# Kernel optimization log

Hardware: AMD Instinct MI355X
Metric: run time of the kernel (lower is better)

The kernel has to match this reference:

```python
import jax, jax.numpy as jnp
import numpy as np

B, N, DIM = 4, 1024, 768
HEADS, DIM_HEAD = 12, 64
INNER = HEADS * DIM_HEAD  # 768
SCALE = DIM ** -0.5


def setup_inputs() -> dict:
    key = jax.random.key(0)
    ks = jax.random.split(key, 5)
    return {
        "x": jax.random.normal(ks[0], (B, N, DIM), dtype=jnp.float32),
        "pos_embedding": jax.random.normal(ks[1], (B, N, DIM), dtype=jnp.float32),
        "w_qkv": jax.random.normal(ks[2], (DIM, 3 * INNER), dtype=jnp.float32) * (DIM ** -0.5),
        "w_qk_pos": jax.random.normal(ks[3], (DIM, 2 * INNER), dtype=jnp.float32) * (DIM ** -0.5),
        "w_out": jax.random.normal(ks[4], (INNER, DIM), dtype=jnp.float32) * (INNER ** -0.5),
        "b_out": jnp.zeros((DIM,), dtype=jnp.float32),
    }


def _split_heads(t):
    # [b, n, h*d] -> [b, h, n, d]
    b, n, _ = t.shape
    return t.reshape(b, n, HEADS, DIM_HEAD).transpose(0, 2, 1, 3)


def reference(x, pos_embedding, w_qkv, w_qk_pos, w_out, b_out):
    qkv = x @ w_qkv  # [b, n, 3*inner]
    q, k, v = (_split_heads(t) for t in jnp.split(qkv, 3, axis=-1))
    qk_pos = pos_embedding @ w_qk_pos  # [b, n, 2*inner]
    q_pos, k_pos = (_split_heads(t) for t in jnp.split(qk_pos, 2, axis=-1))

    dots = jnp.einsum('bhid,bhjd->bhij', q, k) * SCALE
    dots_pos = jnp.einsum('bhid,bhjd->bhij', q_pos, k_pos) * SCALE
    dots = (dots + dots_pos) * 0.5  # averaged content+positional scores

    attn = jax.nn.softmax(dots, axis=-1)
    out = jnp.einsum('bhij,bhjd->bhid', attn, v)
    out = out.transpose(0, 2, 1, 3).reshape(x.shape[0], x.shape[1], INNER)
    return out @ w_out + b_out
```

## Files before the change

### kernel.cpp

```cpp
#include <hip/hip_runtime.h>
#include <cstdint>
#include <cstddef>

typedef __bf16 bf16;
typedef __bf16 bf16x8 __attribute__((ext_vector_type(8)));
typedef __bf16 bf16x4v __attribute__((ext_vector_type(4)));
typedef float  f32x4  __attribute__((ext_vector_type(4)));

#define MFMA(a, b, c) __builtin_amdgcn_mfma_f32_16x16x32_bf16((a), (b), (c), 0, 0, 0)

typedef __attribute__((address_space(3))) unsigned int  lds_u32;
typedef __attribute__((address_space(1))) unsigned int glob_u32;


__global__ void k_prep(const float* __restrict__ x, const float* __restrict__ pos,
                       const float* __restrict__ w_qkv, const float* __restrict__ w_qk_pos,
                       const float* __restrict__ w_out,
                       bf16* __restrict__ xb, bf16* __restrict__ posb,
                       bf16* __restrict__ wqkvT, bf16* __restrict__ wqkposT,
                       bf16* __restrict__ woutT) {
    __shared__ float t[32][33];
    const int blk = blockIdx.x;
    if (blk < 6144) {
        int i = blk * 256 + threadIdx.x;
        const float* in = x; bf16* out = xb;
        if (i >= 786432) { i -= 786432; in = pos; out = posb; }
        float4 v = reinterpret_cast<const float4*>(in)[i];
        bf16x4v o; o[0] = (bf16)v.x; o[1] = (bf16)v.y; o[2] = (bf16)v.z; o[3] = (bf16)v.w;
        reinterpret_cast<bf16x4v*>(out)[i] = o;
        return;
    }
    int bx = (blk - 6144) % 144, ky = (blk - 6144) / 144;
    const float* in; bf16* out; int N;
    if (bx < 72)       { in = w_qkv;    out = wqkvT;   N = 2304; }
    else if (bx < 120) { in = w_qk_pos; out = wqkposT; N = 1536; bx -= 72; }
    else               { in = w_out;    out = woutT;   N = 768;  bx -= 120; }
    const int n0 = bx * 32, k0 = ky * 32;
    const int tx = threadIdx.x & 31, ty = threadIdx.x >> 5;
#pragma unroll
    for (int r = 0; r < 32; r += 8)
        t[ty + r][tx] = in[(size_t)(k0 + ty + r) * N + n0 + tx];
    __syncthreads();
#pragma unroll
    for (int r = 0; r < 32; r += 8)
        out[(size_t)(n0 + ty + r) * 768 + k0 + tx] = (bf16)t[tx][ty + r];
}

__launch_bounds__(512, 2)
__global__ void k_gemm12(const bf16* __restrict__ xb, const bf16* __restrict__ posb,
                         const bf16* __restrict__ wqkvT, const bf16* __restrict__ wqkposT,
                         bf16* __restrict__ qcat, bf16* __restrict__ kcat,
                         bf16* __restrict__ vT) {
    __shared__ bf16 lA[2][2][2][128][32];
    __shared__ bf16 lB[2][2][2][128][32];

    const int tid  = threadIdx.x;
    const int lane = tid & 63, wave = tid >> 6;
    const int quad = lane >> 4, col = lane & 15;
    const int sw2  = (col >> 1) & 3;
    const int rg8  = (quad ^ sw2) * 8;
    const int mh   = wave >> 2;
    const int nh   = (wave >> 1) & 1;
    const int nb64 = (wave & 1) * 64;
    const int wm   = mh * 128, wn = (wave & 3) * 64;

    const int fid = blockIdx.x;
    const int xcd = fid & 7, s = fid >> 3;
    const int bx = s % 15;
    const int by = xcd * 2 + s / 15;

    int mode, nBase;
    const bf16 *A, *BT;
    if (bx < 9) { mode = 0; A = xb;   BT = wqkvT;   nBase = bx * 256; }
    else        { mode = 1; A = posb; BT = wqkposT; nBase = (bx - 9) * 256; }
    const int mBase = by * 256;

    const bf16* Ap = A  + (size_t)mBase * 768;
    const bf16* Bp = BT + (size_t)nBase * 768;

#define STAGE_A8(ss, h, t)                                                     \
    _Pragma("unroll")                                                          \
    for (int j = 0; j < 2; ++j) {                                              \
        int c = (lane & 3) ^ ((lane >> 3) & 3);                                \
        __builtin_amdgcn_global_load_lds(                                      \
            (const glob_u32*)(Ap + (size_t)((h) * 128 + wave * 16 + (lane >> 2)) * 768 \
                              + (t) * 64 + j * 32 + c * 8),                    \
            (lds_u32*)(&lA[ss][h][j][wave * 16][0]), 16, 0, 0);                \
    }
#define STAGE_B8(ss, h, t)                                                     \
    _Pragma("unroll")                                                          \
    for (int j = 0; j < 2; ++j) {                                              \
        int c = (lane & 3) ^ ((lane >> 3) & 3);                                \
        __builtin_amdgcn_global_load_lds(                                      \
            (const glob_u32*)(Bp + (size_t)((h) * 128 + wave * 16 + (lane >> 2)) * 768 \
                              + (t) * 64 + j * 32 + c * 8),                    \
            (lds_u32*)(&lB[ss][h][j][wave * 16][0]), 16, 0, 0);                \
    }

#define READ_A8(ss, mq)                                                        \
    _Pragma("unroll")                                                          \
    for (int f = 0; f < 4; ++f)                                                \
    _Pragma("unroll")                                                          \
    for (int ks = 0; ks < 2; ++ks)                                             \
        afr[f][ks] = *(const bf16x8*)&lA[ss][mh][ks][(mq) * 64 + f * 16 + col][rg8];
#define READ_B8(ss, nq)                                                        \
    _Pragma("unroll")                                                          \
    for (int n = 0; n < 2; ++n)                                                \
    _Pragma("unroll")                                                          \
    for (int ks = 0; ks < 2; ++ks)                                             \
        bfr[n][ks] = *(const bf16x8*)&lB[ss][nh][ks][nb64 + (nq) * 32 + n * 16 + col][rg8];

#define MM16(mq, nq)                                                           \
    __builtin_amdgcn_s_setprio(1);                                             \
    _Pragma("unroll")                                                          \
    for (int ks = 0; ks < 2; ++ks)                                             \
    _Pragma("unroll")                                                          \
    for (int f = 0; f < 4; ++f)                                                \
    _Pragma("unroll")                                                          \
    for (int n = 0; n < 2; ++n)                                                \
        acc[(mq) * 4 + f][(nq) * 2 + n] =                                      \
            MFMA(afr[f][ks], bfr[n][ks], acc[(mq) * 4 + f][(nq) * 2 + n]);     \
    __builtin_amdgcn_s_setprio(0);

#define BAR()   __builtin_amdgcn_s_barrier()
#define LGKM0() do { asm volatile("s_waitcnt lgkmcnt(0)" ::: "memory");        \
                     __builtin_amdgcn_sched_barrier(0); } while (0)

    f32x4 acc[8][4];
#pragma unroll
    for (int mi = 0; mi < 8; ++mi)
#pragma unroll
        for (int ni = 0; ni < 4; ++ni) acc[mi][ni] = f32x4{0.f, 0.f, 0.f, 0.f};

    bf16x8 afr[4][2], bfr[2][2];

    STAGE_A8(0, 0, 0) STAGE_A8(0, 1, 0)
    STAGE_B8(0, 0, 0)
    STAGE_B8(0, 1, 0)
    STAGE_A8(1, 0, 1) STAGE_A8(1, 1, 1)
    asm volatile("s_waitcnt vmcnt(4)" ::: "memory");
    BAR();

    for (int i = 0; i < 6; ++i) {
        const int tO = 2 * i + 1, tE2 = 2 * i + 2, tO2 = 2 * i + 3;
        READ_A8(0, 0) READ_B8(0, 0)
        STAGE_B8(1, 0, tO)
        BAR(); LGKM0();
        MM16(0, 0)
        BAR();
        READ_B8(0, 1)
        STAGE_B8(1, 1, tO)
        BAR(); LGKM0();
        MM16(0, 1)
        BAR();
        READ_A8(0, 1)
        BAR(); LGKM0();
        MM16(1, 1)
        BAR();
        READ_B8(0, 0)
        if (i < 5) { STAGE_A8(0, 0, tE2) STAGE_A8(0, 1, tE2) }
        BAR(); LGKM0();
        MM16(1, 0)
        if (i < 5) { asm volatile("s_waitcnt vmcnt(4)" ::: "memory"); }
        else       { asm volatile("s_waitcnt vmcnt(0)" ::: "memory"); }
        BAR();
        READ_A8(1, 0) READ_B8(1, 0)
        if (i < 5) STAGE_B8(0, 1, tE2)
        BAR(); LGKM0();
        MM16(0, 0)
        BAR();
        READ_B8(1, 1)
        if (i < 5) STAGE_B8(0, 0, tE2)
        BAR(); LGKM0();
        MM16(0, 1)
        BAR();
        READ_A8(1, 1)
        BAR(); LGKM0();
        MM16(1, 1)
        BAR();
        READ_B8(1, 0)
        if (i < 5) { STAGE_A8(1, 0, tO2) STAGE_A8(1, 1, tO2) }
        BAR(); LGKM0();
        MM16(1, 0)
        if (i < 5) { asm volatile("s_waitcnt vmcnt(4)" ::: "memory"); }
        BAR();
    }
#undef STAGE_A8
#undef STAGE_B8
#undef READ_A8
#undef READ_B8
#undef MM16
#undef BAR
#undef LGKM0

    const float c2s = 0.018042195912f * 1.44269504089f;
    const int bb = mBase >> 10;
    const int sr0 = (mBase & 1023) + wm + quad * 4;
    const int which = (mode == 0) ? (nBase >= 1536 ? 2 : (nBase >= 768 ? 1 : 0))
                                  : (nBase >= 768 ? 1 : 0);
#pragma unroll
    for (int ni = 0; ni < 4; ++ni) {
        const int nb = nBase + wn + ni * 16;
        const int rem = nb - which * 768;
        const int hh = rem >> 6, dd0 = rem & 63;
        const size_t hb = (size_t)(bb * 12 + hh);
        if (mode == 0 && which == 2) {
            bf16* dstv = vT + (hb * 64 + dd0 + col) * 1024 + sr0;
#pragma unroll
            for (int mi = 0; mi < 8; ++mi) {
                bf16x4v pk;
#pragma unroll
                for (int r = 0; r < 4; ++r) pk[r] = (bf16)acc[mi][ni][r];
                *(bf16x4v*)(dstv + mi * 16) = pk;
            }
        } else {
            const float scl = (which == 0) ? c2s : 1.0f;
            bf16* dstq = (which == 0 ? qcat : kcat)
                       + (hb * 1024 + sr0) * 128 + (mode == 1 ? 64 : 0) + dd0 + col;
#pragma unroll
            for (int mi = 0; mi < 8; ++mi)
#pragma unroll
                for (int r = 0; r < 4; ++r)
                    dstq[(size_t)(mi * 16 + r) * 128] = (bf16)(acc[mi][ni][r] * scl);
        }
    }
}

__launch_bounds__(256, 3)
__global__ void k_attn(const bf16* __restrict__ qcat, const bf16* __restrict__ kcat,
                       const bf16* __restrict__ vT, bf16* __restrict__ attn_out) {
    __shared__ bf16 lK[2][64][128];
    __shared__ bf16 lV[2][64][72];

    const int tid  = threadIdx.x;
    const int lane = tid & 63, wave = tid >> 6;
    const int quad = lane >> 4, col = lane & 15;
    const int sw   = col & 7;

    const int fid = blockIdx.x;
    const int xcd = fid & 7, s = fid >> 3;
    const int qt = s & 15;
    const int unit = (s >> 4) * 8 + xcd;
    const int b = unit / 12, h = unit % 12;

    const bf16* Qb = qcat + (size_t)unit * 1024 * 128;
    const bf16* Kb = kcat + (size_t)unit * 1024 * 128;
    const bf16* Vb = vT   + (size_t)unit * 64 * 1024;

    const int kidx = wave * 256 + lane;

#define STAGE_K(buf, kv0)                                                      \
    _Pragma("unroll")                                                          \
    for (int j = 0; j < 4; ++j) {                                              \
        int idx = kidx + j * 64;                                               \
        int row = idx >> 4, c = idx & 15, csrc = c ^ (row & 7);                \
        __builtin_amdgcn_global_load_lds(                                      \
            (const glob_u32*)(Kb + (size_t)((kv0) + row) * 128 + csrc * 8),    \
            (lds_u32*)(&lK[buf][0][0] + (wave * 4 + j) * 512), 16, 0, 0);      \
    }

    int vdj[2], vsk[2], vka[2];
#pragma unroll
    for (int j = 0; j < 2; ++j) {
        int cid = wave * 128 + j * 64 + lane;
        vdj[j] = cid >> 3;
        int sck = cid & 7;
        vsk[j] = sck * 8;
        vka[j] = (sck >> 2) * 32 + (sck & 1) * 16 + ((sck >> 1) & 1) * 4;
    }

#define LOAD_V(kv0)                                                            \
    _Pragma("unroll")                                                          \
    for (int j = 0; j < 2; ++j)                                                \
        vreg[j] = *(const uint4*)(Vb + (size_t)vdj[j] * 1024 + (kv0) + vsk[j]);
#define WRITE_V(buf)                                                           \
    _Pragma("unroll")                                                          \
    for (int j = 0; j < 2; ++j) {                                               \
        *(uint2*)&lV[buf][vdj[j]][vka[j]]     = make_uint2(vreg[j].x, vreg[j].y);\
        *(uint2*)&lV[buf][vdj[j]][vka[j] + 8] = make_uint2(vreg[j].z, vreg[j].w);\
    }

    bf16x8 qb[4];
    {
        const bf16* qrow = Qb + (size_t)(qt * 64 + wave * 16 + col) * 128;
#pragma unroll
        for (int f = 0; f < 4; ++f) qb[f] = *(const bf16x8*)(qrow + f * 32 + quad * 8);
    }

    f32x4 o[4];
#pragma unroll
    for (int vt = 0; vt < 4; ++vt) o[vt] = f32x4{0.f, 0.f, 0.f, 0.f};
    float lsum = 0.f;

    uint4 vreg[2];
    STAGE_K(0, 0)
    LOAD_V(0)
    WRITE_V(0)

    for (int it = 0; it < 16; ++it) {
        const int cur = it & 1, nxt = cur ^ 1;
        __syncthreads();
        if (it < 15) {
            const int kv1 = (it + 1) * 64;
            STAGE_K(nxt, kv1)
            LOAD_V(kv1)
        }

        f32x4 st[4];
#pragma unroll
        for (int t = 0; t < 4; ++t) st[t] = f32x4{0.f, 0.f, 0.f, 0.f};
        __builtin_amdgcn_s_setprio(1);
#pragma unroll
        for (int t = 0; t < 4; ++t)
#pragma unroll
            for (int f = 0; f < 4; ++f) {
                bf16x8 kf = *(const bf16x8*)&lK[cur][t * 16 + col][((f * 4 + quad) ^ sw) * 8];
                st[t] = MFMA(kf, qb[f], st[t]);
            }
        __builtin_amdgcn_s_setprio(0);

        bf16x8 pbf[2];
#pragma unroll
        for (int c = 0; c < 2; ++c) {
#pragma unroll
            for (int r = 0; r < 4; ++r) {
                float p0 = exp2f(st[2 * c][r]);
                float p1 = exp2f(st[2 * c + 1][r]);
                lsum += p0 + p1;
                pbf[c][r]     = (bf16)p0;
                pbf[c][4 + r] = (bf16)p1;
            }
        }

        __builtin_amdgcn_s_setprio(1);
#pragma unroll
        for (int c = 0; c < 2; ++c)
#pragma unroll
            for (int vt = 0; vt < 4; ++vt) {
                bf16x8 vf = *(const bf16x8*)&lV[cur][vt * 16 + col][c * 32 + quad * 8];
                o[vt] = MFMA(vf, pbf[c], o[vt]);
            }
        __builtin_amdgcn_s_setprio(0);

        if (it < 15) WRITE_V(nxt)
    }

    float l = lsum;
    l += __shfl_xor(l, 16, 64);
    l += __shfl_xor(l, 32, 64);
    const float inv = 1.f / l;

    const int qrow = qt * 64 + wave * 16 + col;
    bf16* dst = attn_out + ((size_t)b * 1024 + qrow) * 768 + h * 64;
#pragma unroll
    for (int vt = 0; vt < 4; ++vt) {
        bf16x4v pk;
#pragma unroll
        for (int r = 0; r < 4; ++r) pk[r] = (bf16)(o[vt][r] * inv);
        *(bf16x4v*)(dst + vt * 16 + quad * 4) = pk;
    }
#undef STAGE_K
#undef LOAD_V
#undef WRITE_V
}

__launch_bounds__(256, 3)
__global__ void k_gemm_out(const bf16* __restrict__ aout, const bf16* __restrict__ woutT,
                           const float* __restrict__ bias, float* __restrict__ out) {
    __shared__ bf16 lA[2][64][32];
    __shared__ bf16 lB[2][64][32];

    const int tid  = threadIdx.x;
    const int lane = tid & 63, wave = tid >> 6;
    const int quad = lane >> 4, col = lane & 15;
    const int sw2  = (col >> 1) & 3;
    const int wm = (wave >> 1) * 32, wn = (wave & 1) * 32;

    const int fid = blockIdx.x;
    const int xcd = fid & 7, s = fid >> 3;
    const int bx = s % 12;
    const int by = xcd * 8 + s / 12;

    const int mBase = by * 64, nBase = bx * 64;

    const bf16* Ap = aout  + (size_t)mBase * 768;
    const bf16* Bp = woutT + (size_t)nBase * 768;

#define STAGE_O(buf, k0)                                                        \
    {                                                                           \
        int idx = wave * 64 + lane;                                             \
        int row = idx >> 2, c = (idx & 3) ^ ((row >> 1) & 3);                   \
        __builtin_amdgcn_global_load_lds(                                       \
            (const glob_u32*)(Ap + (size_t)row * 768 + (k0) + c * 8),           \
            (lds_u32*)((char*)&lA[buf][0][0] + wave * 1024), 16, 0, 0);         \
        __builtin_amdgcn_global_load_lds(                                       \
            (const glob_u32*)(Bp + (size_t)row * 768 + (k0) + c * 8),           \
            (lds_u32*)((char*)&lB[buf][0][0] + wave * 1024), 16, 0, 0);         \
    }

    f32x4 acc[2][2];
#pragma unroll
    for (int mi = 0; mi < 2; ++mi)
#pragma unroll
        for (int ni = 0; ni < 2; ++ni) acc[mi][ni] = f32x4{0.f, 0.f, 0.f, 0.f};

    STAGE_O(0, 0)
    for (int it = 0; it < 24; ++it) {
        const int cur = it & 1, nxt = cur ^ 1;
        __syncthreads();
        if (it < 23) STAGE_O(nxt, (it + 1) * 32)

        bf16x8 af[2], bfg[2];
#pragma unroll
        for (int mi = 0; mi < 2; ++mi)
            af[mi]  = *(const bf16x8*)&lA[cur][wm + mi * 16 + col][(quad ^ sw2) * 8];
#pragma unroll
        for (int ni = 0; ni < 2; ++ni)
            bfg[ni] = *(const bf16x8*)&lB[cur][wn + ni * 16 + col][(quad ^ sw2) * 8];
#pragma unroll
        for (int mi = 0; mi < 2; ++mi)
#pragma unroll
            for (int ni = 0; ni < 2; ++ni)
                acc[mi][ni] = MFMA(af[mi], bfg[ni], acc[mi][ni]);
    }
#undef STAGE_O

#pragma unroll
    for (int mi = 0; mi < 2; ++mi)
#pragma unroll
        for (int ni = 0; ni < 2; ++ni)
#pragma unroll
            for (int r = 0; r < 4; ++r) {
                int m = mBase + wm + mi * 16 + quad * 4 + r;
                int n = nBase + wn + ni * 16 + col;
                out[(size_t)m * 768 + n] = acc[mi][ni][r] + bias[n];
            }
}

extern "C" void kernel_launch(void* const* d_in, const int* in_sizes, int n_in,
                              void* d_out, int out_size, void* d_ws, size_t ws_size,
                              hipStream_t stream) {
    const float* x        = (const float*)d_in[0];
    const float* pos      = (const float*)d_in[1];
    const float* w_qkv    = (const float*)d_in[2];
    const float* w_qk_pos = (const float*)d_in[3];
    const float* w_out    = (const float*)d_in[4];
    const float* b_out    = (const float*)d_in[5];
    float* out = (float*)d_out;

    char* ws = (char*)d_ws;
    bf16* xb      = (bf16*)(ws);
    bf16* posb    = (bf16*)(ws + 6291456);
    bf16* wqkvT   = (bf16*)(ws + 12582912);
    bf16* wqkposT = (bf16*)(ws + 16121856);
    bf16* woutT   = (bf16*)(ws + 18481152);
    bf16* qcat    = (bf16*)(ws + 19660800);
    bf16* kcat    = (bf16*)(ws + 32243712);
    bf16* vT      = (bf16*)(ws + 44826624);
    bf16* aout    = (bf16*)(ws + 51118080);

    k_prep<<<9600, 256, 0, stream>>>(x, pos, w_qkv, w_qk_pos, w_out,
                                     xb, posb, wqkvT, wqkposT, woutT);
    k_gemm12<<<240, 512, 0, stream>>>(xb, posb, wqkvT, wqkposT, qcat, kcat, vT);
    k_attn<<<768, 256, 0, stream>>>(qcat, kcat, vT, aout);
    k_gemm_out<<<768, 256, 0, stream>>>(aout, woutT, b_out, out);
}
```

Before: 174.4 us.

## Process two 64-row query tiles per attention block to reuse K/V tiles

Each attention workgroup now handles 128 query rows (two sub-tiles per wave) instead of 64, so every K/V tile staged into LDS serves twice as many queries. The grid is halved from 768 to 384 blocks, and the mapping from block index to query tile and head is adjusted to match. This cuts global K/V traffic and LDS staging per query. In exchange it doubles the per-thread registers for accumulators and Q fragments, and leaves fewer blocks to fill the CUs, which may lower occupancy or parallelism.

```diff
diff --git a/kernel.cpp b/kernel.cpp
--- a/kernel.cpp
+++ b/kernel.cpp
@@ -239,8 +239,8 @@
 
     const int fid = blockIdx.x;
     const int xcd = fid & 7, s = fid >> 3;
-    const int qt = s & 15;
-    const int unit = (s >> 4) * 8 + xcd;
+    const int qt = s & 7;
+    const int unit = (s >> 3) * 8 + xcd;
     const int b = unit / 12, h = unit % 12;
 
     const bf16* Qb = qcat + (size_t)unit * 1024 * 128;
@@ -280,17 +280,20 @@
         *(uint2*)&lV[buf][vdj[j]][vka[j] + 8] = make_uint2(vreg[j].z, vreg[j].w);\
     }
 
-    bf16x8 qb[4];
-    {
-        const bf16* qrow = Qb + (size_t)(qt * 64 + wave * 16 + col) * 128;
-#pragma unroll
-        for (int f = 0; f < 4; ++f) qb[f] = *(const bf16x8*)(qrow + f * 32 + quad * 8);
-    }
-
-    f32x4 o[4];
-#pragma unroll
-    for (int vt = 0; vt < 4; ++vt) o[vt] = f32x4{0.f, 0.f, 0.f, 0.f};
-    float lsum = 0.f;
+    bf16x8 qb[2][4];
+#pragma unroll
+    for (int hq = 0; hq < 2; ++hq) {
+        const bf16* qrow = Qb + (size_t)(qt * 128 + hq * 64 + wave * 16 + col) * 128;
+#pragma unroll
+        for (int f = 0; f < 4; ++f) qb[hq][f] = *(const bf16x8*)(qrow + f * 32 + quad * 8);
+    }
+
+    f32x4 o[2][4];
+#pragma unroll
+    for (int hq = 0; hq < 2; ++hq)
+#pragma unroll
+        for (int vt = 0; vt < 4; ++vt) o[hq][vt] = f32x4{0.f, 0.f, 0.f, 0.f};
+    float lsum0 = 0.f, lsum1 = 0.f;
 
     uint4 vreg[2];
     STAGE_K(0, 0)
@@ -306,58 +309,66 @@
             LOAD_V(kv1)
         }
 
-        f32x4 st[4];
-#pragma unroll
-        for (int t = 0; t < 4; ++t) st[t] = f32x4{0.f, 0.f, 0.f, 0.f};
-        __builtin_amdgcn_s_setprio(1);
-#pragma unroll
-        for (int t = 0; t < 4; ++t)
-#pragma unroll
-            for (int f = 0; f < 4; ++f) {
-                bf16x8 kf = *(const bf16x8*)&lK[cur][t * 16 + col][((f * 4 + quad) ^ sw) * 8];
-                st[t] = MFMA(kf, qb[f], st[t]);
+#pragma unroll
+        for (int hq = 0; hq < 2; ++hq) {
+            f32x4 st[4];
+#pragma unroll
+            for (int t = 0; t < 4; ++t) st[t] = f32x4{0.f, 0.f, 0.f, 0.f};
+            __builtin_amdgcn_s_setprio(1);
+#pragma unroll
+            for (int t = 0; t < 4; ++t)
+#pragma unroll
+                for (int f = 0; f < 4; ++f) {
+                    bf16x8 kf = *(const bf16x8*)&lK[cur][t * 16 + col][((f * 4 + quad) ^ sw) * 8];
+                    st[t] = MFMA(kf, qb[hq][f], st[t]);
+                }
+            __builtin_amdgcn_s_setprio(0);
+
+            bf16x8 pbf[2];
+            float ls = 0.f;
+#pragma unroll
+            for (int c = 0; c < 2; ++c) {
+#pragma unroll
+                for (int r = 0; r < 4; ++r) {
+                    float p0 = exp2f(st[2 * c][r]);
+                    float p1 = exp2f(st[2 * c + 1][r]);
+                    ls += p0 + p1;
+                    pbf[c][r]     = (bf16)p0;
+                    pbf[c][4 + r] = (bf16)p1;
+                }
             }
-        __builtin_amdgcn_s_setprio(0);
-
-        bf16x8 pbf[2];
-#pragma unroll
-        for (int c = 0; c < 2; ++c) {
-#pragma unroll
-            for (int r = 0; r < 4; ++r) {
-                float p0 = exp2f(st[2 * c][r]);
-                float p1 = exp2f(st[2 * c + 1][r]);
-                lsum += p0 + p1;
-                pbf[c][r]     = (bf16)p0;
-                pbf[c][4 + r] = (bf16)p1;
-            }
+            if (hq == 0) lsum0 += ls; else lsum1 += ls;
+
+            __builtin_amdgcn_s_setprio(1);
+#pragma unroll
+            for (int c = 0; c < 2; ++c)
+#pragma unroll
+                for (int vt = 0; vt < 4; ++vt) {
+                    bf16x8 vf = *(const bf16x8*)&lV[cur][vt * 16 + col][c * 32 + quad * 8];
+                    o[hq][vt] = MFMA(vf, pbf[c], o[hq][vt]);
+                }
+            __builtin_amdgcn_s_setprio(0);
         }
 
-        __builtin_amdgcn_s_setprio(1);
-#pragma unroll
-        for (int c = 0; c < 2; ++c)
-#pragma unroll
-            for (int vt = 0; vt < 4; ++vt) {
-                bf16x8 vf = *(const bf16x8*)&lV[cur][vt * 16 + col][c * 32 + quad * 8];
-                o[vt] = MFMA(vf, pbf[c], o[vt]);
-            }
-        __builtin_amdgcn_s_setprio(0);
-
         if (it < 15) WRITE_V(nxt)
     }
 
-    float l = lsum;
-    l += __shfl_xor(l, 16, 64);
-    l += __shfl_xor(l, 32, 64);
-    const float inv = 1.f / l;
-
-    const int qrow = qt * 64 + wave * 16 + col;
-    bf16* dst = attn_out + ((size_t)b * 1024 + qrow) * 768 + h * 64;
-#pragma unroll
-    for (int vt = 0; vt < 4; ++vt) {
-        bf16x4v pk;
-#pragma unroll
-        for (int r = 0; r < 4; ++r) pk[r] = (bf16)(o[vt][r] * inv);
-        *(bf16x4v*)(dst + vt * 16 + quad * 4) = pk;
+#pragma unroll
+    for (int hq = 0; hq < 2; ++hq) {
+        float l = (hq == 0) ? lsum0 : lsum1;
+        l += __shfl_xor(l, 16, 64);
+        l += __shfl_xor(l, 32, 64);
+        const float inv = 1.f / l;
+
+        const int qrow = qt * 128 + hq * 64 + wave * 16 + col;
+        bf16* dst = attn_out + ((size_t)b * 1024 + qrow) * 768 + h * 64;
+#pragma unroll
+        for (int vt = 0; vt < 4; ++vt) {
+            bf16x4v pk;
+#pragma unroll
+            for (int r = 0; r < 4; ++r) pk[r] = (bf16)(o[hq][vt][r] * inv);
+            *(bf16x4v*)(dst + vt * 16 + quad * 4) = pk;
+        }
     }
 #undef STAGE_K
 #undef LOAD_V
@@ -462,6 +473,6 @@
     k_prep<<<9600, 256, 0, stream>>>(x, pos, w_qkv, w_qk_pos, w_out,
                                      xb, posb, wqkvT, wqkposT, woutT);
     k_gemm12<<<240, 512, 0, stream>>>(xb, posb, wqkvT, wqkposT, qcat, kcat, vT);
-    k_attn<<<768, 256, 0, stream>>>(qcat, kcat, vT, aout);
+    k_attn<<<384, 256, 0, stream>>>(qcat, kcat, vT, aout);
     k_gemm_out<<<768, 256, 0, stream>>>(aout, woutT, b_out, out);
 }
```

After: 182.6 us. 1.05x slower.
